# Kernel optimization log

Measured on AMD Instinct MI355X. Metric: run time of the kernel, lower is better.

Reference implementation:

```python
import jax, jax.numpy as jnp
import numpy as np

B, N = 128, 512            # graphs per batch, nodes (seq len) per graph
NODE_VOCAB, APP_VOCAB = 30000, 5000
D, R, K = 128, 512, 3      # embed_size, rec_embed dim, Chebyshev order
EPS = 1e-12


def setup_inputs() -> dict:
    key = jax.random.key(0)
    ks = jax.random.split(key, 8)
    return {
        # all tokens nonzero -> every position is a valid node (item > 0 filter passes)
        "input_seq": jax.random.randint(ks[0], (B, N), 1, NODE_VOCAB),
        "recd_token": jax.random.randint(ks[1], (B, N), 1, APP_VOCAB),
        "embed_table": jax.random.normal(ks[2], (NODE_VOCAB, D), jnp.float32) * 0.02,
        "rec_embed_table": jax.random.normal(ks[3], (APP_VOCAB, R), jnp.float32) * 0.02,
        "cheb_w1": jax.random.normal(ks[4], (K, D, D), jnp.float32) / np.sqrt(D),
        "cheb_b1": jnp.zeros((D,), jnp.float32),
        "cheb_w2": jax.random.normal(ks[5], (K, D, D), jnp.float32) / np.sqrt(D),
        "cheb_b2": jnp.zeros((D,), jnp.float32),
    }


def _prop_matrix(app_emb):
    """Per-sample scaled Laplacian L_hat = -D^{-1/2} A D^{-1/2}.

    app_emb: [B,N,R] (detached upstream, matching recd.detach() in the source).
    Adjacency: cosine-sim matrix, entries below the mean of the nonzero strict
    upper triangle zeroed. ChebConv receives edge_index only -> binary weights,
    self-loops removed, default lambda_max=2 -> L_hat = -A_norm.
    """
    app_feat = app_emb / jnp.maximum(
        jnp.linalg.norm(app_emb, axis=-1, keepdims=True), EPS)      # F.normalize dim=1
    A = jnp.einsum('bnr,bmr->bnm', app_feat, app_feat)              # [B,N,N]
    upper = jnp.triu(A, 1)
    cnt = jnp.sum(upper != 0, axis=(1, 2)).astype(A.dtype)
    mean = jnp.sum(upper, axis=(1, 2)) / jnp.maximum(cnt, 1.0)      # [B]
    A = jnp.where(A < mean[:, None, None], 0.0, A)
    adj = (A != 0).astype(A.dtype) * (1.0 - jnp.eye(N, dtype=A.dtype))  # binary, no self-loops
    deg = adj.sum(-1)                                               # [B,N]
    dinv = jnp.where(deg > 0, jax.lax.rsqrt(jnp.maximum(deg, EPS)), 0.0)
    return -(dinv[:, :, None] * adj * dinv[:, None, :])             # [B,N,N]


def _cheb(x, S, w, b):
    # Chebyshev recurrence T0=x, T1=Sx, T2=2S T1 - T0
    tx0 = x
    tx1 = jnp.einsum('bnm,bmd->bnd', S, tx0)
    tx2 = 2.0 * jnp.einsum('bnm,bmd->bnd', S, tx1) - tx0
    return (jnp.einsum('bnd,de->bne', tx0, w[0])
            + jnp.einsum('bnd,de->bne', tx1, w[1])
            + jnp.einsum('bnd,de->bne', tx2, w[2]) + b)


def reference(input_seq, recd_token, embed_table, rec_embed_table,
              cheb_w1, cheb_b1, cheb_w2, cheb_b2):
    app_emb = rec_embed_table[recd_token]                           # [B,N,R]
    # adjacency built from detached embeddings (recd.detach() in source)
    S = jax.lax.stop_gradient(_prop_matrix(jax.lax.stop_gradient(app_emb)))
    x = embed_table[input_seq]                                      # [B,N,D]
    x = jax.nn.relu(_cheb(x, S, cheb_w1, cheb_b1))
    x = jax.nn.relu(_cheb(x, S, cheb_w2, cheb_b2))
    out = jnp.concatenate([x, app_emb], axis=-1)                    # [B,N,D+R]
    return out.reshape(B * N, D + R)                                # Batch'ed node features
```

## Files before the change

kernel.cpp:

```cpp
#include <hip/hip_runtime.h>
#include <hip/hip_bf16.h>

typedef __attribute__((ext_vector_type(8))) unsigned short ushort8;
typedef __attribute__((ext_vector_type(4))) unsigned short bf16x4;
typedef __attribute__((ext_vector_type(8))) short short8;
typedef __attribute__((ext_vector_type(4))) float f32x4;
typedef __attribute__((ext_vector_type(2))) unsigned long long u64x2;

#define DEV __device__ __forceinline__

DEV unsigned short f2bf(float f) {
    unsigned u = __builtin_bit_cast(unsigned, f);
    return (unsigned short)((u + 0x7fffu + ((u >> 16) & 1u)) >> 16);
}
DEV float bf2f(unsigned short h) {
    unsigned u = ((unsigned)h) << 16;
    return __builtin_bit_cast(float, u);
}
DEV float wred(float v) {
#pragma unroll
    for (int m = 32; m > 0; m >>= 1) v += __shfl_xor(v, m, 64);
    return v;
}

constexpr int N_ = 512, D_ = 128, R_ = 512;
constexpr long NN2 = (long)N_ * N_;
constexpr int PSTR = 520;
constexpr int USTR = 136;

DEV void gll16(const void* g, void* l) {
    __builtin_amdgcn_global_load_lds(
        (const __attribute__((address_space(1))) unsigned*)g,
        (__attribute__((address_space(3))) unsigned*)l, 16, 0, 0);
}


__global__ __launch_bounds__(256) void k_front(const int* __restrict__ recd,
                                               const float* __restrict__ rtab,
                                               const int* __restrict__ seq,
                                               const float* __restrict__ etab,
                                               const float* __restrict__ w1,
                                               const float* __restrict__ w2,
                                               float* __restrict__ out,
                                               unsigned short* __restrict__ x,
                                               unsigned short* __restrict__ wT,
                                               unsigned short* __restrict__ rtb,
                                               float* __restrict__ rnorm) {
    int bid = blockIdx.x, tid = threadIdx.x;
    if (bid < 16384) {
        int lane = tid & 63, w = tid >> 6;
        long r = (long)bid * 4 + w;
        int tok = recd[r];
        const float* src = rtab + (long)tok * R_;
        int j = lane * 8;
        float4 v0 = *(const float4*)(src + j);
        float4 v1 = *(const float4*)(src + j + 4);
        float ssq = v0.x*v0.x + v0.y*v0.y + v0.z*v0.z + v0.w*v0.w
                  + v1.x*v1.x + v1.y*v1.y + v1.z*v1.z + v1.w*v1.w;
        ssq = wred(ssq);
        float* o = out + r * 640 + 128 + j;
        *(float4*)o = v0;
        *(float4*)(o + 4) = v1;
        if (lane == 0) rnorm[r] = 1.0f / fmaxf(sqrtf(ssq), 1e-12f);
    } else if (bid < 20480) {
        long e8 = ((long)(bid - 16384) * 256 + tid) * 8;
        long r = e8 >> 7;
        int d0 = (int)(e8 & 127);
        int tok = seq[r];
        const float* src = etab + (long)tok * D_ + d0;
        float4 v0 = *(const float4*)src, v1 = *(const float4*)(src + 4);
        ushort8 u;
        u[0]=f2bf(v0.x); u[1]=f2bf(v0.y); u[2]=f2bf(v0.z); u[3]=f2bf(v0.w);
        u[4]=f2bf(v1.x); u[5]=f2bf(v1.y); u[6]=f2bf(v1.z); u[7]=f2bf(v1.w);
        *(ushort8*)(x + e8) = u;
    } else if (bid < 20864) {
        int o = (bid - 20480) * 256 + tid;
        int l = o / 49152;
        int rr = o - l * 49152;
        int mat = rr >> 14;
        int e2 = rr & 16383;
        int e = e2 >> 7, d = e2 & 127;
        const float* w = l ? w2 : w1;
        float v;
        if (mat == 0)      v = w[d * 128 + e] - w[32768 + d * 128 + e];
        else if (mat == 1) v = w[16384 + d * 128 + e];
        else               v = 2.0f * w[32768 + d * 128 + e];
        wT[o] = f2bf(v);
    } else {
        long e8 = ((long)(bid - 20864) * 256 + tid) * 8;
        float4 v0 = *(const float4*)(rtab + e8), v1 = *(const float4*)(rtab + e8 + 4);
        ushort8 u;
        u[0]=f2bf(v0.x); u[1]=f2bf(v0.y); u[2]=f2bf(v0.z); u[3]=f2bf(v0.w);
        u[4]=f2bf(v1.x); u[5]=f2bf(v1.y); u[6]=f2bf(v1.z); u[7]=f2bf(v1.w);
        *(ushort8*)(rtb + e8) = u;
    }
}


DEV void stage_rowmajor(const unsigned short* base, long ld, int k0,
                        unsigned short* dst, int tid) {
#pragma unroll
    for (int i = 0; i < 4; ++i) {
        int u = i * 256 + tid;
        int r = u >> 3, c = (u & 7) * 8;
        gll16(base + (long)r * ld + k0 + c,
              dst + i * 2048 + (tid & 448) * 8);
    }
}

DEV void stage_gather(const unsigned short* tab, const int* toks, int k0,
                      unsigned short* dst, int tid) {
#pragma unroll
    for (int i = 0; i < 4; ++i) {
        int u = i * 256 + tid;
        int r = u >> 3, c = (u & 7) * 8;
        gll16(tab + (long)toks[r] * 512 + k0 + c,
              dst + i * 2048 + (tid & 448) * 8);
    }
}


DEV void stageA256(const unsigned short* base, int k0, unsigned short* dst, int tid) {
    int w = tid >> 6;
#pragma unroll
    for (int i = 0; i < 4; ++i) {
        int u = i * 512 + tid;
        int r = u >> 3, c = (u & 7) * 8;
        gll16(base + (long)r * 128 + k0 + c, dst + (i * 64 + w * 8) * 64);
    }
}

DEV void stageB128(const unsigned short* base, int k0, unsigned short* dst, int tid) {
    int w = tid >> 6;
#pragma unroll
    for (int i = 0; i < 2; ++i) {
        int u = i * 512 + tid;
        int r = u >> 3, c = (u & 7) * 8;
        gll16(base + (long)r * 128 + k0 + c, dst + (i * 64 + w * 8) * 64);
    }
}


__global__ __launch_bounds__(256) void k_adj(const unsigned short* __restrict__ rtb,
                                             const int* __restrict__ recd,
                                             const float* __restrict__ rnorm,
                                             unsigned short* __restrict__ Abf,
                                             float* __restrict__ psum,
                                             float* __restrict__ pcnt) {
    __shared__ __align__(16) unsigned short As[128 * 64], Bs[128 * 64];
    __shared__ int toks[256];
    __shared__ float sred[4], cred[4];
    int g = blockIdx.x;
    int r8 = g & 7, q = g >> 3;
    int q10 = q / 10;
    int b = r8 + (q10 << 3);
    int t = q - q10 * 10;
    int tm = (t < 4) ? 0 : (t < 7) ? 1 : (t < 9) ? 2 : 3;
    int tn = t - (tm * (9 - tm)) / 2 + tm;
    bool diag = (tm == tn);
    int tid = threadIdx.x, lane = tid & 63, wave = tid >> 6;
    if (tid < 128) toks[tid] = recd[b * 512 + tm * 128 + tid];
    else           toks[tid] = recd[b * 512 + tn * 128 + (tid - 128)];
    int wm = wave >> 1, wn = wave & 1;
    int fr = lane & 15, ko = (lane >> 4) * 8;
    f32x4 acc[4][4] = {};
    for (int k0 = 0; k0 < 512; k0 += 64) {
        __syncthreads();
        stage_gather(rtb, toks, k0, As, tid);
        if (!diag) stage_gather(rtb, toks + 128, k0, Bs, tid);
        __syncthreads();
        const unsigned short* Bsrc = diag ? As : Bs;
#pragma unroll
        for (int ks = 0; ks < 2; ++ks) {
            short8 a[4], bb[4];
#pragma unroll
            for (int m = 0; m < 4; ++m)
                a[m] = *(const short8*)(As + (wm * 64 + m * 16 + fr) * 64 + ks * 32 + ko);
#pragma unroll
            for (int n = 0; n < 4; ++n)
                bb[n] = *(const short8*)(Bsrc + (wn * 64 + n * 16 + fr) * 64 + ks * 32 + ko);
#pragma unroll
            for (int m = 0; m < 4; ++m)
#pragma unroll
                for (int n = 0; n < 4; ++n)
                    acc[m][n] = __builtin_amdgcn_mfma_f32_16x16x32_bf16(
                        a[m], bb[n], acc[m][n], 0, 0, 0);
        }
    }
    float s = 0.f, c = 0.f;
    unsigned short* Ab = Abf + (long)b * NN2;
    const float* rnb = rnorm + (long)b * 512;
#pragma unroll
    for (int m = 0; m < 4; ++m) {
        int gi0 = tm * 128 + wm * 64 + m * 16 + (lane >> 4) * 4;
        float4 rni = *(const float4*)(rnb + gi0);
#pragma unroll
        for (int n = 0; n < 4; ++n) {
            int gj = tn * 128 + wn * 64 + n * 16 + fr;
            float rj = rnb[gj];
            f32x4 v = acc[m][n];
            bf16x4 tw;
#pragma unroll
            for (int qq = 0; qq < 4; ++qq) {
                int gi = gi0 + qq;
                float vv = v[qq] * (&rni.x)[qq] * rj;
                unsigned short bv = f2bf(vv);
                Ab[(long)gi * N_ + gj] = bv;
                tw[qq] = bv;
                if (gj > gi) {
                    s += vv;
                    c += (vv != 0.0f) ? 1.0f : 0.0f;
                }
            }
            if (!diag)
                *(bf16x4*)(Ab + (long)gj * N_ + gi0) = tw;
        }
    }
    s = wred(s);
    c = wred(c);
    if (lane == 0) { sred[wave] = s; cred[wave] = c; }
    __syncthreads();
    if (tid == 0) {
        psum[b * 16 + t] = sred[0] + sred[1] + sred[2] + sred[3];
        pcnt[b * 16 + t] = cred[0] + cred[1] + cred[2] + cred[3];
    }
}

__global__ __launch_bounds__(256) void k_degtrs(unsigned short* __restrict__ Abf,
                                                const float* __restrict__ psum,
                                                const float* __restrict__ pcnt,
                                                const unsigned short* __restrict__ xin,
                                                float* __restrict__ dinv,
                                                unsigned short* __restrict__ pT) {
    __shared__ unsigned char mb[4][64];
    __shared__ float sdinv[64];
    __shared__ unsigned short t[64 * 128];
    int bid = blockIdx.x;
    int q = bid >> 3, r8 = bid & 7;
    int b = r8 + ((q >> 3) << 3);
    int tn = q & 7;
    int tid = threadIdx.x, lane = tid & 63, w = tid >> 6;
    float s = 0.f, c = 0.f;
#pragma unroll
    for (int k = 0; k < 10; ++k) { s += psum[b * 16 + k]; c += pcnt[b * 16 + k]; }
    float m = s / fmaxf(c, 1.0f);
#pragma unroll 1
    for (int i = 0; i < 16; ++i) {
        int rl = w * 16 + i;
        long r = (long)b * 512 + tn * 64 + rl;
        int ig = tn * 64 + rl;
        ushort8 v = *(const ushort8*)(Abf + r * 512 + lane * 8);
        unsigned byt = 0;
        int cnt = 0;
#pragma unroll
        for (int k = 0; k < 8; ++k) {
            float f = bf2f(v[k]);
            int j = lane * 8 + k;
            bool keep = (f >= m) && (f != 0.0f) && (j != ig);
            byt |= (keep ? 1u : 0u) << k;
            cnt += keep ? 1 : 0;
        }
        mb[w][lane] = (unsigned char)byt;
        float fc = wred((float)cnt);
        if (lane < 8) {
            unsigned long long mword = *(const unsigned long long*)&mb[w][lane * 8];
            *(unsigned long long*)((unsigned char*)Abf + r * 1024 + lane * 8) = mword;
        }
        if (lane == 8) {
            float dv = (fc > 0.f) ? rsqrtf(fc) : 0.f;
            dinv[r] = dv;
            sdinv[rl] = dv;
        }
    }
    __syncthreads();
    const unsigned short* ib = xin + ((long)b * 512 + tn * 64) * 128;
    unsigned short* ob = pT + (long)b * 65536 + tn * 64;
#pragma unroll
    for (int i = 0; i < 4; ++i) {
        int u = i * 256 + tid;
        int n = u >> 4, g = u & 15;
        float sc = sdinv[n];
        ushort8 v = *(const ushort8*)(ib + n * 128 + g * 8);
        ushort8 sv;
#pragma unroll
        for (int tt = 0; tt < 8; ++tt) sv[tt] = f2bf(bf2f(v[tt]) * sc);
        int gs = g ^ ((n >> 3) & 7);
        *(ushort8*)(t + n * 128 + gs * 8) = sv;
    }
    __syncthreads();
#pragma unroll
    for (int i = 0; i < 4; ++i) {
        int u = i * 256 + tid;
        int d = u >> 3, n8 = (u & 7) * 8;
        ushort8 v;
#pragma unroll
        for (int tt = 0; tt < 8; ++tt) {
            int n = n8 + tt;
            int g = (d >> 3) ^ ((n >> 3) & 7);
            v[tt] = t[n * 128 + g * 8 + (d & 7)];
        }
        *(ushort8*)(ob + (long)d * 512 + n8) = v;
    }
}

__global__ __launch_bounds__(512) void k_sxm(const unsigned short* __restrict__ Abf,
                                             const float* __restrict__ dinv,
                                             const unsigned short* __restrict__ pT,
                                             unsigned short* __restrict__ outN,
                                             unsigned short* __restrict__ outT) {
    __shared__ __align__(16) unsigned short Ps[128 * PSTR];
    __shared__ __align__(8) unsigned short lut4[16 * 4];
    int tid = threadIdx.x, lane = tid & 63, w = tid >> 6;
    if (tid < 16) {
        unsigned long long e = 0;
#pragma unroll
        for (int j = 0; j < 4; ++j)
            if ((tid >> j) & 1) e |= 0x3F80ull << (16 * j);
        *(unsigned long long*)(lut4 + tid * 4) = e;
    }
    int g = blockIdx.x;
    int xcd = g & 7, idx = g >> 3;
    int b = xcd + ((idx >> 1) << 3);
    int half = idx & 1;
    int wm = w >> 1, wn = w & 1;
    int fr = lane & 15, ko = (lane >> 4) * 8;
    const unsigned char* mbase = (const unsigned char*)Abf + (long)b * 524288;
    const unsigned short* pb = pT + (long)b * 65536;
#pragma unroll
    for (int i = 0; i < 16; ++i) {
        int r = i * 8 + w;
        gll16(pb + (long)r * 512 + lane * 8, Ps + r * PSTR);
    }
    __syncthreads();
    f32x4 acc[4][4] = {};
    int rowbase = half * 256 + wm * 64;
#pragma unroll 1
    for (int k0 = 0; k0 < 512; k0 += 128) {
        u64x2 mw[4];
#pragma unroll
        for (int m = 0; m < 4; ++m) {
            int row = rowbase + m * 16 + fr;
            mw[m] = *(const u64x2*)(mbase + (long)row * 1024 + (k0 >> 3));
        }
#pragma unroll
        for (int kss = 0; kss < 4; ++kss) {
            short8 a4[4], b4[4];
#pragma unroll
            for (int m = 0; m < 4; ++m) {
                unsigned w32 = (unsigned)(mw[m][kss >> 1] >> ((kss & 1) * 32));
                unsigned byt = (w32 >> ko) & 255u;
                unsigned long long lo = *(const unsigned long long*)(lut4 + (byt & 15u) * 4);
                unsigned long long hi = *(const unsigned long long*)(lut4 + (byt >> 4) * 4);
                u64x2 tt; tt[0] = lo; tt[1] = hi;
                a4[m] = __builtin_bit_cast(short8, tt);
            }
#pragma unroll
            for (int n = 0; n < 4; ++n)
                b4[n] = *(const short8*)(Ps + (wn * 64 + n * 16 + fr) * PSTR + k0 + kss * 32 + ko);
            __builtin_amdgcn_s_setprio(1);
#pragma unroll
            for (int m = 0; m < 4; ++m)
#pragma unroll
                for (int n = 0; n < 4; ++n)
                    acc[m][n] = __builtin_amdgcn_mfma_f32_16x16x32_bf16(
                        a4[m], b4[n], acc[m][n], 0, 0, 0);
            __builtin_amdgcn_s_setprio(0);
        }
    }
    unsigned short* on = outN + (long)b * 65536;
#pragma unroll
    for (int m = 0; m < 4; ++m) {
        int gi0 = half * 256 + wm * 64 + m * 16 + ((lane >> 4) << 2);
        float4 dv = *(const float4*)(dinv + (long)b * 512 + gi0);
#pragma unroll
        for (int n = 0; n < 4; ++n) {
            int gj = wn * 64 + n * 16 + fr;
            bf16x4 tw;
#pragma unroll
            for (int qq = 0; qq < 4; ++qq) {
                float dq = (&dv.x)[qq];
                float t1v = -dq * acc[m][n][qq];
                on[(long)(gi0 + qq) * 128 + gj] = f2bf(t1v);
                tw[qq] = f2bf(dq * t1v);
            }
            *(bf16x4*)(outT + (long)b * 65536 + (long)gj * 512 + gi0) = tw;
        }
    }
}

template <int LAYER>
__global__ __launch_bounds__(512) void k_sxp(const unsigned short* __restrict__ Abf,
                                             const float* __restrict__ dinv,
                                             const unsigned short* __restrict__ pTin,
                                             const unsigned short* __restrict__ t0,
                                             const unsigned short* __restrict__ t1,
                                             const unsigned short* __restrict__ wTl,
                                             const float* __restrict__ bias,
                                             unsigned short* __restrict__ ybf,
                                             unsigned short* __restrict__ pTout,
                                             float* __restrict__ out) {
    __shared__ __align__(16) unsigned short lds[128 * PSTR];
    __shared__ __align__(8) unsigned short lut4[16 * 4];
    int tid = threadIdx.x, lane = tid & 63, w = tid >> 6;
    if (tid < 16) {
        unsigned long long e = 0;
#pragma unroll
        for (int j = 0; j < 4; ++j)
            if ((tid >> j) & 1) e |= 0x3F80ull << (16 * j);
        *(unsigned long long*)(lut4 + tid * 4) = e;
    }
    int g = blockIdx.x;
    int xcd = g & 7, idx = g >> 3;
    int b = xcd + ((idx >> 1) << 3);
    int half = idx & 1;
    int wm = w >> 1, wn = w & 1;
    int fr = lane & 15, ko = (lane >> 4) * 8;
    unsigned short* As  = lds;
    unsigned short* Bs  = lds + 16384;
    unsigned short* uL  = lds + 24576;
    {
        const unsigned char* mbase = (const unsigned char*)Abf + (long)b * 524288;
        const unsigned short* pb = pTin + (long)b * 65536;
#pragma unroll
        for (int i = 0; i < 16; ++i) {
            int r = i * 8 + w;
            gll16(pb + (long)r * 512 + lane * 8, lds + r * PSTR);
        }
        __syncthreads();
        f32x4 acc[4][4] = {};
        int rowbase = half * 256 + wm * 64;
#pragma unroll 1
        for (int k0 = 0; k0 < 512; k0 += 128) {
            u64x2 mw[4];
#pragma unroll
            for (int m = 0; m < 4; ++m) {
                int row = rowbase + m * 16 + fr;
                mw[m] = *(const u64x2*)(mbase + (long)row * 1024 + (k0 >> 3));
            }
#pragma unroll
            for (int kss = 0; kss < 4; ++kss) {
                short8 a4[4], b4[4];
#pragma unroll
                for (int m = 0; m < 4; ++m) {
                    unsigned w32 = (unsigned)(mw[m][kss >> 1] >> ((kss & 1) * 32));
                    unsigned byt = (w32 >> ko) & 255u;
                    unsigned long long lo = *(const unsigned long long*)(lut4 + (byt & 15u) * 4);
                    unsigned long long hi = *(const unsigned long long*)(lut4 + (byt >> 4) * 4);
                    u64x2 tt; tt[0] = lo; tt[1] = hi;
                    a4[m] = __builtin_bit_cast(short8, tt);
                }
#pragma unroll
                for (int n = 0; n < 4; ++n)
                    b4[n] = *(const short8*)(lds + (wn * 64 + n * 16 + fr) * PSTR + k0 + kss * 32 + ko);
                __builtin_amdgcn_s_setprio(1);
#pragma unroll
                for (int m = 0; m < 4; ++m)
#pragma unroll
                    for (int n = 0; n < 4; ++n)
                        acc[m][n] = __builtin_amdgcn_mfma_f32_16x16x32_bf16(
                            a4[m], b4[n], acc[m][n], 0, 0, 0);
                __builtin_amdgcn_s_setprio(0);
            }
        }
        __syncthreads();
#pragma unroll
        for (int m = 0; m < 4; ++m) {
            int li0 = wm * 64 + m * 16 + ((lane >> 4) << 2);
            float4 dv = *(const float4*)(dinv + (long)b * 512 + half * 256 + li0);
#pragma unroll
            for (int n = 0; n < 4; ++n) {
                int gj = wn * 64 + n * 16 + fr;
#pragma unroll
                for (int qq = 0; qq < 4; ++qq)
                    uL[(li0 + qq) * USTR + gj] = f2bf(-(&dv.x)[qq] * acc[m][n][qq]);
            }
        }
    }
    long row0 = (long)b * 512 + half * 256;
    f32x4 acc2[4][4] = {};
#pragma unroll 1
    for (int mat = 0; mat < 2; ++mat) {
        const unsigned short* tsrc = (mat == 0) ? (t0 + row0 * D_) : (t1 + row0 * D_);
        const unsigned short* wsrc = wTl + mat * 16384;
#pragma unroll 1
        for (int k0 = 0; k0 < 128; k0 += 64) {
            __syncthreads();
            stageA256(tsrc, k0, As, tid);
            stageB128(wsrc, k0, Bs, tid);
            __syncthreads();
#pragma unroll
            for (int ks = 0; ks < 2; ++ks) {
                short8 a[4], bfr[4];
#pragma unroll
                for (int m = 0; m < 4; ++m)
                    a[m] = *(const short8*)(As + (wm * 64 + m * 16 + fr) * 64 + ks * 32 + ko);
#pragma unroll
                for (int n = 0; n < 4; ++n)
                    bfr[n] = *(const short8*)(Bs + (wn * 64 + n * 16 + fr) * 64 + ks * 32 + ko);
#pragma unroll
                for (int m = 0; m < 4; ++m)
#pragma unroll
                    for (int n = 0; n < 4; ++n)
                        acc2[m][n] = __builtin_amdgcn_mfma_f32_16x16x32_bf16(
                            a[m], bfr[n], acc2[m][n], 0, 0, 0);
            }
        }
    }
#pragma unroll 1
    for (int s2 = 0; s2 < 2; ++s2) {
        __syncthreads();
        stageB128(wTl + 32768, s2 * 64, Bs, tid);
        __syncthreads();
#pragma unroll
        for (int ks = 0; ks < 2; ++ks) {
            short8 a[4], bfr[4];
#pragma unroll
            for (int m = 0; m < 4; ++m)
                a[m] = *(const short8*)(uL + (wm * 64 + m * 16 + fr) * USTR + s2 * 64 + ks * 32 + ko);
#pragma unroll
            for (int n = 0; n < 4; ++n)
                bfr[n] = *(const short8*)(Bs + (wn * 64 + n * 16 + fr) * 64 + ks * 32 + ko);
#pragma unroll
            for (int m = 0; m < 4; ++m)
#pragma unroll
                for (int n = 0; n < 4; ++n)
                    acc2[m][n] = __builtin_amdgcn_mfma_f32_16x16x32_bf16(
                        a[m], bfr[n], acc2[m][n], 0, 0, 0);
        }
    }
#pragma unroll
    for (int m = 0; m < 4; ++m) {
        long gr0 = row0 + wm * 64 + m * 16 + ((lane >> 4) << 2);
        float4 dv;
        if (LAYER == 1) dv = *(const float4*)(dinv + gr0);
#pragma unroll
        for (int n = 0; n < 4; ++n) {
            int gj = wn * 64 + n * 16 + (lane & 15);
            bf16x4 tw;
#pragma unroll
            for (int qq = 0; qq < 4; ++qq) {
                long gr = gr0 + qq;
                float v = fmaxf(acc2[m][n][qq] + bias[gj], 0.0f);
                if (LAYER == 1) {
                    ybf[gr * D_ + gj] = f2bf(v);
                    tw[qq] = f2bf((&dv.x)[qq] * v);
                } else {
                    out[gr * 640 + gj] = v;
                }
            }
            if (LAYER == 1)
                *(bf16x4*)(pTout + (gr0 >> 9) * 65536 + (long)gj * 512 + (gr0 & 511)) = tw;
        }
    }
}


extern "C" void kernel_launch(void* const* d_in, const int* in_sizes, int n_in,
                              void* d_out, int out_size, void* d_ws, size_t ws_size,
                              hipStream_t stream) {
    const int* seq    = (const int*)d_in[0];
    const int* recd   = (const int*)d_in[1];
    const float* etab = (const float*)d_in[2];
    const float* rtab = (const float*)d_in[3];
    const float* w1   = (const float*)d_in[4];
    const float* b1   = (const float*)d_in[5];
    const float* w2   = (const float*)d_in[6];
    const float* b2   = (const float*)d_in[7];
    float* out = (float*)d_out;
    char* ws = (char*)d_ws;

    if (ws_size < 151470592u) return;

    unsigned short* Abf  = (unsigned short*)(ws);
    unsigned short* pTa  = (unsigned short*)(ws + 67108864);
    unsigned short* pTb  = (unsigned short*)(ws + 83886080);
    unsigned short* t1   = (unsigned short*)(ws + 100663296);
    unsigned short* rtb  = (unsigned short*)(ws + 117440512);
    float* rnorm         = (float*)(ws + 122683392);
    unsigned short* xbf  = (unsigned short*)(ws + 134217728);
    unsigned short* wT   = (unsigned short*)(ws + 150994944);
    float* psum = (float*)(ws + 151191552);
    float* pcnt = (float*)(ws + 151199744);
    float* dinv = (float*)(ws + 151208448);

    k_front<<<22114, 256, 0, stream>>>(recd, rtab, seq, etab, w1, w2,
                                       out, xbf, wT, rtb, rnorm);
    k_adj<<<1280, 256, 0, stream>>>(rtb, recd, rnorm, Abf, psum, pcnt);
    k_degtrs<<<1024, 256, 0, stream>>>(Abf, psum, pcnt, xbf, dinv, pTa);
    k_sxm<<<256, 512, 0, stream>>>(Abf, dinv, pTa, t1, pTb);
    k_sxp<1><<<256, 512, 0, stream>>>(Abf, dinv, pTb, xbf, t1, wT, b1,
                                      xbf, pTa, nullptr);
    k_sxm<<<256, 512, 0, stream>>>(Abf, dinv, pTa, t1, pTb);
    k_sxp<2><<<256, 512, 0, stream>>>(Abf, dinv, pTb, xbf, t1, wT + 49152, b2,
                                      nullptr, nullptr, out);
}
```

Measured before the change: 221.2 us.

## Enlarge adjacency Gram tiles to 256x256 with 512-thread blocks

The cosine-similarity kernel now computes each per-graph upper-triangular Gram matrix as three 256x256 tiles instead of ten 128x128 tiles. Each block has 8 waves holding 8x4 MFMA accumulators, gather token indices are hoisted into registers, and the MFMA loop is bracketed with s_setprio. The goal is to cut redundant gathers of embedding rows and raise MFMA arithmetic intensity per staged byte. In exchange the grid shrinks from 1280 to 384 blocks, the shared-memory footprint doubles, and the diagonal tiles do more redundant lower-triangle work, all of which may hurt occupancy.

After: 237.9 us. 7.6% more time.

```diff
diff --git a/kernel.cpp b/kernel.cpp
--- a/kernel.cpp
+++ b/kernel.cpp
@@ -97,29 +97,6 @@
 }
 
 
-DEV void stage_rowmajor(const unsigned short* base, long ld, int k0,
-                        unsigned short* dst, int tid) {
-#pragma unroll
-    for (int i = 0; i < 4; ++i) {
-        int u = i * 256 + tid;
-        int r = u >> 3, c = (u & 7) * 8;
-        gll16(base + (long)r * ld + k0 + c,
-              dst + i * 2048 + (tid & 448) * 8);
-    }
-}
-
-DEV void stage_gather(const unsigned short* tab, const int* toks, int k0,
-                      unsigned short* dst, int tid) {
-#pragma unroll
-    for (int i = 0; i < 4; ++i) {
-        int u = i * 256 + tid;
-        int r = u >> 3, c = (u & 7) * 8;
-        gll16(tab + (long)toks[r] * 512 + k0 + c,
-              dst + i * 2048 + (tid & 448) * 8);
-    }
-}
-
-
 DEV void stageA256(const unsigned short* base, int k0, unsigned short* dst, int tid) {
     int w = tid >> 6;
 #pragma unroll
@@ -141,62 +118,82 @@
 }
 
 
-__global__ __launch_bounds__(256) void k_adj(const unsigned short* __restrict__ rtb,
+__global__ __launch_bounds__(512) void k_adj(const unsigned short* __restrict__ rtb,
                                              const int* __restrict__ recd,
                                              const float* __restrict__ rnorm,
                                              unsigned short* __restrict__ Abf,
                                              float* __restrict__ psum,
                                              float* __restrict__ pcnt) {
-    __shared__ __align__(16) unsigned short As[128 * 64], Bs[128 * 64];
-    __shared__ int toks[256];
-    __shared__ float sred[4], cred[4];
+    __shared__ __align__(16) unsigned short As[256 * 64], Bs[256 * 64];
+    __shared__ int toks[512];
+    __shared__ float sred[8], cred[8];
     int g = blockIdx.x;
-    int r8 = g & 7, q = g >> 3;
-    int q10 = q / 10;
-    int b = r8 + (q10 << 3);
-    int t = q - q10 * 10;
-    int tm = (t < 4) ? 0 : (t < 7) ? 1 : (t < 9) ? 2 : 3;
-    int tn = t - (tm * (9 - tm)) / 2 + tm;
-    bool diag = (tm == tn);
-    int tid = threadIdx.x, lane = tid & 63, wave = tid >> 6;
-    if (tid < 128) toks[tid] = recd[b * 512 + tm * 128 + tid];
-    else           toks[tid] = recd[b * 512 + tn * 128 + (tid - 128)];
-    int wm = wave >> 1, wn = wave & 1;
+    int xcd = g & 7, q = g >> 3;
+    int q3 = q / 3;
+    int b = xcd + (q3 << 3);
+    int t = q - q3 * 3;
+    int tm = (t == 2) ? 1 : 0;
+    int tn = (t == 0) ? 0 : 1;
+    bool diag = (t != 1);
+    int tid = threadIdx.x, lane = tid & 63, w = tid >> 6;
+    if (tid < 256) toks[tid] = recd[b * 512 + tm * 256 + tid];
+    else           toks[tid] = recd[b * 512 + tn * 256 + (tid - 256)];
+    int wm = w >> 2, wn = w & 3;
     int fr = lane & 15, ko = (lane >> 4) * 8;
-    f32x4 acc[4][4] = {};
+    __syncthreads();
+    int tokA[4], tokB[4];
+#pragma unroll
+    for (int i = 0; i < 4; ++i) {
+        int r = (i * 512 + tid) >> 3;
+        tokA[i] = toks[r];
+        tokB[i] = toks[256 + r];
+    }
+    f32x4 acc[8][4] = {};
     for (int k0 = 0; k0 < 512; k0 += 64) {
         __syncthreads();
-        stage_gather(rtb, toks, k0, As, tid);
-        if (!diag) stage_gather(rtb, toks + 128, k0, Bs, tid);
+#pragma unroll
+        for (int i = 0; i < 4; ++i) {
+            int c = ((i * 512 + tid) & 7) * 8;
+            gll16(rtb + (long)tokA[i] * 512 + k0 + c, As + (i * 64 + w * 8) * 64);
+        }
+        if (!diag) {
+#pragma unroll
+            for (int i = 0; i < 4; ++i) {
+                int c = ((i * 512 + tid) & 7) * 8;
+                gll16(rtb + (long)tokB[i] * 512 + k0 + c, Bs + (i * 64 + w * 8) * 64);
+            }
+        }
         __syncthreads();
         const unsigned short* Bsrc = diag ? As : Bs;
 #pragma unroll
         for (int ks = 0; ks < 2; ++ks) {
-            short8 a[4], bb[4];
-#pragma unroll
-            for (int m = 0; m < 4; ++m)
-                a[m] = *(const short8*)(As + (wm * 64 + m * 16 + fr) * 64 + ks * 32 + ko);
+            short8 a[8], bb[4];
+#pragma unroll
+            for (int m = 0; m < 8; ++m)
+                a[m] = *(const short8*)(As + (wm * 128 + m * 16 + fr) * 64 + ks * 32 + ko);
 #pragma unroll
             for (int n = 0; n < 4; ++n)
                 bb[n] = *(const short8*)(Bsrc + (wn * 64 + n * 16 + fr) * 64 + ks * 32 + ko);
-#pragma unroll
-            for (int m = 0; m < 4; ++m)
+            __builtin_amdgcn_s_setprio(1);
+#pragma unroll
+            for (int m = 0; m < 8; ++m)
 #pragma unroll
                 for (int n = 0; n < 4; ++n)
                     acc[m][n] = __builtin_amdgcn_mfma_f32_16x16x32_bf16(
                         a[m], bb[n], acc[m][n], 0, 0, 0);
+            __builtin_amdgcn_s_setprio(0);
         }
     }
     float s = 0.f, c = 0.f;
     unsigned short* Ab = Abf + (long)b * NN2;
     const float* rnb = rnorm + (long)b * 512;
 #pragma unroll
-    for (int m = 0; m < 4; ++m) {
-        int gi0 = tm * 128 + wm * 64 + m * 16 + (lane >> 4) * 4;
+    for (int m = 0; m < 8; ++m) {
+        int gi0 = tm * 256 + wm * 128 + m * 16 + (lane >> 4) * 4;
         float4 rni = *(const float4*)(rnb + gi0);
 #pragma unroll
         for (int n = 0; n < 4; ++n) {
-            int gj = tn * 128 + wn * 64 + n * 16 + fr;
+            int gj = tn * 256 + wn * 64 + n * 16 + fr;
             float rj = rnb[gj];
             f32x4 v = acc[m][n];
             bf16x4 tw;
@@ -218,11 +215,14 @@
     }
     s = wred(s);
     c = wred(c);
-    if (lane == 0) { sred[wave] = s; cred[wave] = c; }
+    if (lane == 0) { sred[w] = s; cred[w] = c; }
     __syncthreads();
     if (tid == 0) {
-        psum[b * 16 + t] = sred[0] + sred[1] + sred[2] + sred[3];
-        pcnt[b * 16 + t] = cred[0] + cred[1] + cred[2] + cred[3];
+        float ss = 0.f, cc = 0.f;
+#pragma unroll
+        for (int i = 0; i < 8; ++i) { ss += sred[i]; cc += cred[i]; }
+        psum[b * 16 + t] = ss;
+        pcnt[b * 16 + t] = cc;
     }
 }
 
@@ -242,7 +242,7 @@
     int tid = threadIdx.x, lane = tid & 63, w = tid >> 6;
     float s = 0.f, c = 0.f;
 #pragma unroll
-    for (int k = 0; k < 10; ++k) { s += psum[b * 16 + k]; c += pcnt[b * 16 + k]; }
+    for (int k = 0; k < 3; ++k) { s += psum[b * 16 + k]; c += pcnt[b * 16 + k]; }
     float m = s / fmaxf(c, 1.0f);
 #pragma unroll 1
     for (int i = 0; i < 16; ++i) {
@@ -585,7 +585,7 @@
 
     k_front<<<22114, 256, 0, stream>>>(recd, rtab, seq, etab, w1, w2,
                                        out, xbf, wT, rtb, rnorm);
-    k_adj<<<1280, 256, 0, stream>>>(rtb, recd, rnorm, Abf, psum, pcnt);
+    k_adj<<<384, 512, 0, stream>>>(rtb, recd, rnorm, Abf, psum, pcnt);
     k_degtrs<<<1024, 256, 0, stream>>>(Abf, psum, pcnt, xbf, dinv, pTa);
     k_sxm<<<256, 512, 0, stream>>>(Abf, dinv, pTa, t1, pTb);
     k_sxp<1><<<256, 512, 0, stream>>>(Abf, dinv, pTb, xbf, t1, wT, b1,
```
